# Optimization experiments

Hardware: AMD Instinct MI355X
Metric: run time of the kernel (lower is better)

Reference implementation:

```python
import jax, jax.numpy as jnp
from jax import lax
import numpy as np

B, T, U, V = 8, 200, 50, 1024  # acts label axis is U+1
BLANK = 0


def setup_inputs() -> dict:
    key = jax.random.key(0)
    k1, k2, k3, k4 = jax.random.split(key, 4)
    acts = jax.random.normal(k1, (B, T, U + 1, V), dtype=jnp.float32)
    labels = jax.random.randint(k2, (B, U), 1, V)          # non-blank targets
    act_lens = jax.random.randint(k3, (B,), T // 2, T + 1).astype(jnp.int32)
    label_lens = jax.random.randint(k4, (B,), U // 2, U + 1).astype(jnp.int32)
    return {"acts": acts, "labels": labels, "act_lens": act_lens, "label_lens": label_lens}


def _rnnt_loss(acts, labels, act_lens, label_lens):
    # acts: (B,T,U+1,V) raw logits -> log-softmax over vocab
    logp = jax.nn.log_softmax(acts, axis=-1)
    lp_blank = logp[..., BLANK]                                   # (B,T,U+1)
    idx = labels[:, None, :, None]                                # (B,1,U,1) broadcasts over T
    lp_emit = jnp.take_along_axis(logp[:, :, :U, :], idx, axis=-1)[..., 0]  # (B,T,U)

    # alpha[t,u] = logaddexp(alpha[t-1,u]+blank(t-1,u), alpha[t,u-1]+emit(t,u-1))
    # row t=0: pure emissions along u
    alpha0 = jnp.concatenate(
        [jnp.zeros((B, 1), logp.dtype), jnp.cumsum(lp_emit[:, 0, :], axis=1)], axis=1
    )  # (B,U+1)

    def t_step(prev_row, inp):
        blank_prev, emit_t = inp                 # (B,U+1), (B,U)
        from_top = prev_row + blank_prev         # contribution from t-1
        def u_step(c, xs):                       # serial left-to-right in u
            ft, em = xs                          # (B,), (B,)
            c = jnp.logaddexp(ft, c + em)
            return c, c
        c0 = from_top[:, 0]
        _, rest = lax.scan(u_step, c0, (from_top[:, 1:].T, emit_t.T))  # (U,B)
        new_row = jnp.concatenate([c0[:, None], rest.T], axis=1)       # (B,U+1)
        return new_row, new_row

    blank_rows = jnp.swapaxes(lp_blank, 0, 1)    # (T,B,U+1)
    emit_rows = jnp.swapaxes(lp_emit, 0, 1)      # (T,B,U)
    _, later_rows = lax.scan(t_step, alpha0, (blank_rows[:-1], emit_rows[1:]))
    alphas = jnp.concatenate([alpha0[None], later_rows], axis=0)       # (T,B,U+1)

    b = jnp.arange(B)
    tl = act_lens - 1
    ul = label_lens
    log_like = alphas[tl, b, ul] + lp_blank[b, tl, ul]  # final blank emission
    return -jnp.sum(log_like)  # size_average=False -> summed cost


def reference(acts, labels, act_lens, label_lens):
    return _rnnt_loss(acts, labels, act_lens, label_lens)
```

## Files before the change

kernel.cpp:

```cpp
#include <hip/hip_runtime.h>
#include <math.h>

#define BB 8
#define TT 200
#define UU 50
#define VV 1024
#define U1 (UU + 1)
#define NROWS (BB * TT * U1)

#define LOG2E 1.44269504088896340736f
#define LN2   0.69314718055994530942f

__device__ __forceinline__ float wave_shr1(float x) {
    int xi = __builtin_bit_cast(int, x);
    int r  = __builtin_amdgcn_update_dpp(0, xi, 0x138, 0xF, 0xF, true);
    return __builtin_bit_cast(float, r);
}

__global__ __launch_bounds__(256) void k_logp(const float* __restrict__ acts,
                                              const int* __restrict__ labels,
                                              float* __restrict__ lpb,
                                              float* __restrict__ lpe) {
    const int wave = threadIdx.x >> 6;
    const int lane = threadIdx.x & 63;
    const int row  = blockIdx.x * 4 + wave;

    int b   = row / (TT * U1);
    int rem = row - b * (TT * U1);
    int t   = rem / U1;
    int u   = rem - t * U1;
    int lab = (u < UU) ? labels[b * UU + u] : 0;

    const float4* p = (const float4*)(acts + (size_t)row * VV);
    float4 v0 = p[lane];
    float4 v1 = p[64 + lane];
    float4 v2 = p[128 + lane];
    float4 v3 = p[192 + lane];

    float m = fmaxf(fmaxf(fmaxf(v0.x, v0.y), fmaxf(v0.z, v0.w)),
                    fmaxf(fmaxf(v1.x, v1.y), fmaxf(v1.z, v1.w)));
    m = fmaxf(m, fmaxf(fmaxf(fmaxf(v2.x, v2.y), fmaxf(v2.z, v2.w)),
                       fmaxf(fmaxf(v3.x, v3.y), fmaxf(v3.z, v3.w))));
#pragma unroll
    for (int s = 1; s < 64; s <<= 1) m = fmaxf(m, __shfl_xor(m, s, 64));

    float sum = __expf(v0.x - m) + __expf(v0.y - m) + __expf(v0.z - m) + __expf(v0.w - m)
              + __expf(v1.x - m) + __expf(v1.y - m) + __expf(v1.z - m) + __expf(v1.w - m)
              + __expf(v2.x - m) + __expf(v2.y - m) + __expf(v2.z - m) + __expf(v2.w - m)
              + __expf(v3.x - m) + __expf(v3.y - m) + __expf(v3.z - m) + __expf(v3.w - m);
#pragma unroll
    for (int s = 1; s < 64; s <<= 1) sum += __shfl_xor(sum, s, 64);

    float logZ = m + __logf(sum);

    int cidx = lab >> 8, lidx = (lab >> 2) & 63, eidx = lab & 3;
    float4 vs = (cidx == 0) ? v0 : (cidx == 1) ? v1 : (cidx == 2) ? v2 : v3;
    float alab = (eidx & 2) ? ((eidx & 1) ? vs.w : vs.z)
                            : ((eidx & 1) ? vs.y : vs.x);
    if (u < UU && lane == lidx) lpe[(b * TT + t) * UU + u] = alab - logZ;
    if (lane == 0)              lpb[row] = v0.x - logZ;
}

__global__ __launch_bounds__(256) void k_dp(const float* __restrict__ lpb,
                                            const float* __restrict__ lpe,
                                            const int* __restrict__ act_lens,
                                            const int* __restrict__ label_lens,
                                            float* __restrict__ loglike) {
    __shared__ __align__(16) float s_lpb[TT * U1];
    __shared__ __align__(16) float s_lpe[TT * UU];

    const int b = blockIdx.x;
    const float4* gb4 = (const float4*)(lpb + (size_t)b * TT * U1);
    const float4* ge4 = (const float4*)(lpe + (size_t)b * TT * UU);
    float4* sb4 = (float4*)s_lpb;
    float4* se4 = (float4*)s_lpe;
    for (int i = threadIdx.x; i < TT * U1 / 4; i += 256) {
        float4 v = gb4[i];
        v.x *= LOG2E; v.y *= LOG2E; v.z *= LOG2E; v.w *= LOG2E;
        sb4[i] = v;
    }
    for (int i = threadIdx.x; i < TT * UU / 4; i += 256) {
        float4 v = ge4[i];
        v.x *= LOG2E; v.y *= LOG2E; v.z *= LOG2E; v.w *= LOG2E;
        se4[i] = v;
    }
    __syncthreads();
    if (threadIdx.x >= 64) return;

    const int u  = threadIdx.x;
    const int uc = min(u, UU);
    const int tl = act_lens[b] - 1;
    const int ul = label_lens[b];
    const int dtgt = tl + ul;
    const float NEG = -INFINITY;
    const float bsave = s_lpb[tl * U1 + ul];

    float Aprev = (u == 0) ? 0.0f : NEG;
    float saved = (dtgt == 0 && u == 0) ? bsave : NEG;

#pragma unroll 5
    for (int d = 1; d <= TT - 1 + UU; ++d) {
        float Aup = wave_shr1(Aprev);
        int t  = d - u;
        int tb = min(max(t - 1, 0), TT - 1);
        int te = min(max(t, 0), TT - 1);
        float bv = s_lpb[tb * U1 + uc];
        float ev = s_lpe[te * UU + max(uc - 1, 0)];
        bool cellok = (t >= 0) & (t < TT) & (u <= UU);
        float ft = (cellok & (t >= 1)) ? Aprev + bv : NEG;
        float em = (cellok & (u >= 1)) ? Aup + ev   : NEG;
        float mm = fmaxf(ft, em);
        float dd = fminf(ft, em) - mm;
        float A  = mm + __builtin_amdgcn_logf(1.0f + __builtin_amdgcn_exp2f(dd));
        A = cellok ? A : NEG;
        saved = (d == dtgt && u == ul) ? A + bsave : saved;
        Aprev = A;
    }
    if (u == ul) loglike[b] = saved * LN2;
}

__global__ void k_sum(const float* __restrict__ loglike, float* __restrict__ out) {
    if (threadIdx.x == 0) {
        float s = 0.0f;
        for (int i = 0; i < BB; ++i) s += loglike[i];
        out[0] = -s;
    }
}

extern "C" void kernel_launch(void* const* d_in, const int* in_sizes, int n_in,
                              void* d_out, int out_size, void* d_ws, size_t ws_size,
                              hipStream_t stream) {
    const float* acts       = (const float*)d_in[0];
    const int*   labels     = (const int*)d_in[1];
    const int*   act_lens   = (const int*)d_in[2];
    const int*   label_lens = (const int*)d_in[3];

    float* ws  = (float*)d_ws;
    float* lpb = ws;
    float* lpe = lpb + NROWS;
    float* ll  = lpe + BB * TT * UU;
    float* out = (float*)d_out;

    k_logp<<<NROWS / 4, 256, 0, stream>>>(acts, labels, lpb, lpe);
    k_dp<<<BB, 256, 0, stream>>>(lpb, lpe, act_lens, label_lens, ll);
    k_sum<<<1, 64, 0, stream>>>(ll, out);
}
```

Baseline: 80.67 us.

## Process two rows per wave, use nontemporal loads, fuse final sum into DP kernel

The log-softmax kernel now handles two vocab rows per wave with nontemporal vector loads, halving the grid and giving each wave more loads in flight. The DP kernel uses 1024 threads for the shared-memory staging and unrolls the diagonal loop further. The separate sum kernel is removed: the last finishing DP block, found through an atomic counter reset in the first kernel, reduces the per-batch log-likelihoods and writes the output. This saves one launch but adds atomics and a reliance on ordering across kernels through the counter.

New measurement: 93.92 us. 1.16x slower.

```diff
diff --git a/kernel.cpp b/kernel.cpp
--- a/kernel.cpp
+++ b/kernel.cpp
@@ -11,78 +11,96 @@
 #define LOG2E 1.44269504088896340736f
 #define LN2   0.69314718055994530942f
 
+typedef float f4v __attribute__((ext_vector_type(4)));
+
 __device__ __forceinline__ float wave_shr1(float x) {
     int xi = __builtin_bit_cast(int, x);
     int r  = __builtin_amdgcn_update_dpp(0, xi, 0x138, 0xF, 0xF, true);
     return __builtin_bit_cast(float, r);
 }
 
-__global__ __launch_bounds__(256) void k_logp(const float* __restrict__ acts,
-                                              const int* __restrict__ labels,
-                                              float* __restrict__ lpb,
-                                              float* __restrict__ lpe) {
-    const int wave = threadIdx.x >> 6;
-    const int lane = threadIdx.x & 63;
-    const int row  = blockIdx.x * 4 + wave;
-
-    int b   = row / (TT * U1);
-    int rem = row - b * (TT * U1);
-    int t   = rem / U1;
-    int u   = rem - t * U1;
-    int lab = (u < UU) ? labels[b * UU + u] : 0;
-
-    const float4* p = (const float4*)(acts + (size_t)row * VV);
-    float4 v0 = p[lane];
-    float4 v1 = p[64 + lane];
-    float4 v2 = p[128 + lane];
-    float4 v3 = p[192 + lane];
-
+__device__ __forceinline__ float rowlogZ(f4v v0, f4v v1, f4v v2, f4v v3) {
     float m = fmaxf(fmaxf(fmaxf(v0.x, v0.y), fmaxf(v0.z, v0.w)),
                     fmaxf(fmaxf(v1.x, v1.y), fmaxf(v1.z, v1.w)));
     m = fmaxf(m, fmaxf(fmaxf(fmaxf(v2.x, v2.y), fmaxf(v2.z, v2.w)),
                        fmaxf(fmaxf(v3.x, v3.y), fmaxf(v3.z, v3.w))));
 #pragma unroll
     for (int s = 1; s < 64; s <<= 1) m = fmaxf(m, __shfl_xor(m, s, 64));
-
     float sum = __expf(v0.x - m) + __expf(v0.y - m) + __expf(v0.z - m) + __expf(v0.w - m)
               + __expf(v1.x - m) + __expf(v1.y - m) + __expf(v1.z - m) + __expf(v1.w - m)
               + __expf(v2.x - m) + __expf(v2.y - m) + __expf(v2.z - m) + __expf(v2.w - m)
               + __expf(v3.x - m) + __expf(v3.y - m) + __expf(v3.z - m) + __expf(v3.w - m);
 #pragma unroll
     for (int s = 1; s < 64; s <<= 1) sum += __shfl_xor(sum, s, 64);
-
-    float logZ = m + __logf(sum);
-
-    int cidx = lab >> 8, lidx = (lab >> 2) & 63, eidx = lab & 3;
-    float4 vs = (cidx == 0) ? v0 : (cidx == 1) ? v1 : (cidx == 2) ? v2 : v3;
-    float alab = (eidx & 2) ? ((eidx & 1) ? vs.w : vs.z)
-                            : ((eidx & 1) ? vs.y : vs.x);
-    if (u < UU && lane == lidx) lpe[(b * TT + t) * UU + u] = alab - logZ;
-    if (lane == 0)              lpb[row] = v0.x - logZ;
+    return m + __logf(sum);
 }
 
-__global__ __launch_bounds__(256) void k_dp(const float* __restrict__ lpb,
-                                            const float* __restrict__ lpe,
-                                            const int* __restrict__ act_lens,
-                                            const int* __restrict__ label_lens,
-                                            float* __restrict__ loglike) {
+__device__ __forceinline__ float pick(f4v v0, f4v v1, f4v v2, f4v v3, int lab) {
+    int cidx = lab >> 8, eidx = lab & 3;
+    f4v vs = (cidx == 0) ? v0 : (cidx == 1) ? v1 : (cidx == 2) ? v2 : v3;
+    return (eidx & 2) ? ((eidx & 1) ? vs.w : vs.z) : ((eidx & 1) ? vs.y : vs.x);
+}
+
+__global__ __launch_bounds__(256) void k_logp(const float* __restrict__ acts,
+                                              const int* __restrict__ labels,
+                                              float* __restrict__ lpb,
+                                              float* __restrict__ lpe,
+                                              int* __restrict__ counter) {
+    if (blockIdx.x == 0 && threadIdx.x == 0) *counter = 0;
+    const int wave = threadIdx.x >> 6;
+    const int lane = threadIdx.x & 63;
+    const int r0   = (blockIdx.x * 4 + wave) * 2;
+    const int r1   = r0 + 1;
+
+    int b0 = r0 / (TT * U1); int rem0 = r0 - b0 * (TT * U1);
+    int t0 = rem0 / U1;      int u0   = rem0 - t0 * U1;
+    int b1 = r1 / (TT * U1); int rem1 = r1 - b1 * (TT * U1);
+    int t1 = rem1 / U1;      int u1   = rem1 - t1 * U1;
+    int lab0 = (u0 < UU) ? labels[b0 * UU + u0] : 0;
+    int lab1 = (u1 < UU) ? labels[b1 * UU + u1] : 0;
+
+    const f4v* p0 = (const f4v*)(acts + (size_t)r0 * VV);
+    const f4v* p1 = (const f4v*)(acts + (size_t)r1 * VV);
+    f4v a0 = __builtin_nontemporal_load(p0 + lane);
+    f4v a1 = __builtin_nontemporal_load(p0 + 64 + lane);
+    f4v a2 = __builtin_nontemporal_load(p0 + 128 + lane);
+    f4v a3 = __builtin_nontemporal_load(p0 + 192 + lane);
+    f4v c0 = __builtin_nontemporal_load(p1 + lane);
+    f4v c1 = __builtin_nontemporal_load(p1 + 64 + lane);
+    f4v c2 = __builtin_nontemporal_load(p1 + 128 + lane);
+    f4v c3 = __builtin_nontemporal_load(p1 + 192 + lane);
+
+    float z0 = rowlogZ(a0, a1, a2, a3);
+    float z1 = rowlogZ(c0, c1, c2, c3);
+
+    int l0 = (lab0 >> 2) & 63, l1 = (lab1 >> 2) & 63;
+    if (u0 < UU && lane == l0) lpe[(b0 * TT + t0) * UU + u0] = pick(a0,a1,a2,a3,lab0) - z0;
+    if (u1 < UU && lane == l1) lpe[(b1 * TT + t1) * UU + u1] = pick(c0,c1,c2,c3,lab1) - z1;
+    if (lane == 0) { lpb[r0] = a0.x - z0; lpb[r1] = c0.x - z1; }
+}
+
+__global__ __launch_bounds__(1024) void k_dp(const float* __restrict__ lpb,
+                                             const float* __restrict__ lpe,
+                                             const int* __restrict__ act_lens,
+                                             const int* __restrict__ label_lens,
+                                             float* __restrict__ loglike,
+                                             int* __restrict__ counter,
+                                             float* __restrict__ out) {
     __shared__ __align__(16) float s_lpb[TT * U1];
     __shared__ __align__(16) float s_lpe[TT * UU];
 
     const int b = blockIdx.x;
-    const float4* gb4 = (const float4*)(lpb + (size_t)b * TT * U1);
-    const float4* ge4 = (const float4*)(lpe + (size_t)b * TT * UU);
-    float4* sb4 = (float4*)s_lpb;
-    float4* se4 = (float4*)s_lpe;
-    for (int i = threadIdx.x; i < TT * U1 / 4; i += 256) {
-        float4 v = gb4[i];
-        v.x *= LOG2E; v.y *= LOG2E; v.z *= LOG2E; v.w *= LOG2E;
-        sb4[i] = v;
+    const f4v* gb4 = (const f4v*)(lpb + (size_t)b * TT * U1);
+    const f4v* ge4 = (const f4v*)(lpe + (size_t)b * TT * UU);
+    f4v* sb4 = (f4v*)s_lpb;
+    f4v* se4 = (f4v*)s_lpe;
+    for (int i = threadIdx.x; i < TT * U1 / 4; i += 1024) {
+        f4v v = gb4[i];
+        sb4[i] = v * LOG2E;
     }
-    for (int i = threadIdx.x; i < TT * UU / 4; i += 256) {
-        float4 v = ge4[i];
-        v.x *= LOG2E; v.y *= LOG2E; v.z *= LOG2E; v.w *= LOG2E;
-        se4[i] = v;
+    for (int i = threadIdx.x; i < TT * UU / 4; i += 1024) {
+        f4v v = ge4[i];
+        se4[i] = v * LOG2E;
     }
     __syncthreads();
     if (threadIdx.x >= 64) return;
@@ -98,7 +116,7 @@
     float Aprev = (u == 0) ? 0.0f : NEG;
     float saved = (dtgt == 0 && u == 0) ? bsave : NEG;
 
-#pragma unroll 5
+#pragma unroll 10
     for (int d = 1; d <= TT - 1 + UU; ++d) {
         float Aup = wave_shr1(Aprev);
         int t  = d - u;
@@ -116,14 +134,20 @@
         saved = (d == dtgt && u == ul) ? A + bsave : saved;
         Aprev = A;
     }
-    if (u == ul) loglike[b] = saved * LN2;
-}
 
-__global__ void k_sum(const float* __restrict__ loglike, float* __restrict__ out) {
-    if (threadIdx.x == 0) {
-        float s = 0.0f;
-        for (int i = 0; i < BB; ++i) s += loglike[i];
-        out[0] = -s;
+    int old = 0;
+    if (u == ul) {
+        atomicExch(&loglike[b], saved * LN2);
+        __threadfence();
+        old = atomicAdd(counter, 1);
+    }
+    old = __shfl(old, ul, 64);
+    if (old == BB - 1) {
+        __threadfence();
+        float v = (u < BB) ? atomicAdd(&loglike[u], 0.0f) : 0.0f;
+#pragma unroll
+        for (int s = 1; s < 8; s <<= 1) v += __shfl_xor(v, s, 64);
+        if (u == 0) out[0] = -v;
     }
 }
 
@@ -139,9 +163,9 @@
     float* lpb = ws;
     float* lpe = lpb + NROWS;
     float* ll  = lpe + BB * TT * UU;
+    int*   cnt = (int*)(ll + BB);
     float* out = (float*)d_out;
 
-    k_logp<<<NROWS / 4, 256, 0, stream>>>(acts, labels, lpb, lpe);
-    k_dp<<<BB, 256, 0, stream>>>(lpb, lpe, act_lens, label_lens, ll);
-    k_sum<<<1, 64, 0, stream>>>(ll, out);
+    k_logp<<<NROWS / 8, 256, 0, stream>>>(acts, labels, lpb, lpe, cnt);
+    k_dp<<<BB, 1024, 0, stream>>>(lpb, lpe, act_lens, label_lens, ll, cnt, out);
 }
```
